# Performance work log

Hardware: AMD Instinct MI355X
Metric: run time of the kernel (lower is better)

Reference implementation:

```python
import jax, jax.numpy as jnp
import numpy as np

# camera / renderer constants (match init_kwargs)
H_IMG, W_IMG = 720, 1280
RR = 2
HS, WS = H_IMG // RR, W_IMG // RR  # 360, 640 ray grid
FX, FY, CX, CY = 600.0, 600.0, 640.0, 360.0
NEAR, FAR = 0.0, 1.5
NS = 10            # N_samples
SHARP = 1000.0
TAU = 100.0
N_SQ = 8
SQRT3 = 3.0 ** 0.5
EPS = 1e-6


def _make_rays():
    # replicates DepthRenderer.get_ray_points with identity camera_pose
    lw = jnp.linspace(0.0, W_IMG - 1, WS)
    lh = jnp.linspace(0.0, H_IMG - 1, HS)
    i, j = jnp.meshgrid(lw, lh)  # 'xy' indexing -> (HS, WS), i varies along width
    dirs = jnp.stack([(i - CX) / FX, -(j - CY) / FY, -jnp.ones_like(i)], -1)
    dirs = dirs / jnp.linalg.norm(dirs, axis=-1, keepdims=True)
    # camera_pose R = I, then right-multiplied by diag(1,-1,-1) in __init__
    R_flip = jnp.diag(jnp.array([1.0, -1.0, -1.0], jnp.float32))
    rays_d = jnp.einsum('hwk,jk->hwj', dirs, R_flip)
    rays_d = rays_d / jnp.linalg.norm(rays_d, axis=-1, keepdims=True)
    rays_o = jnp.zeros(3, jnp.float32)
    return rays_d.astype(jnp.float32), rays_o


def setup_inputs() -> dict:
    key = jax.random.key(0)
    k1, k2, k3, k4, k5 = jax.random.split(key, 5)
    rays_d, rays_o = _make_rays()
    t = jnp.linspace(-1.0, 1.0, NS).astype(jnp.float32)
    # random valid rotations via QR (det fixed to +1; 3x3 so global sign flip negates det)
    A = jax.random.normal(k1, (N_SQ, 3, 3))
    Q, _ = jnp.linalg.qr(A)
    Q = Q * jnp.sign(jnp.linalg.det(Q))[:, None, None]
    pos_xy = jax.random.uniform(k2, (N_SQ, 2), minval=-0.3, maxval=0.3)
    pos_z = jax.random.uniform(k3, (N_SQ, 1), minval=0.5, maxval=1.2)
    pos = jnp.concatenate([pos_xy, pos_z], -1)
    poses = jnp.tile(jnp.eye(4, dtype=jnp.float32)[None], (N_SQ, 1, 1))
    poses = poses.at[:, :3, :3].set(Q).at[:, :3, 3].set(pos)
    sizes = jax.random.uniform(k4, (N_SQ, 3), minval=0.05, maxval=0.15)
    eps12 = jax.random.uniform(k5, (N_SQ, 2), minval=0.3, maxval=1.5)
    params = jnp.concatenate([sizes, eps12], -1).astype(jnp.float32)
    return {"sq_poses": poses.astype(jnp.float32), "sq_params": params,
            "rays_d": rays_d, "rays_o": rays_o, "t": t}


def _sq_F(loc, params):
    # superquadric inside-outside function; F == 1 on the surface
    a = params[:, 0:3][:, None, None, None, :]        # (n,1,1,1,3)
    e1 = params[:, 3][:, None, None, None]
    e2 = params[:, 4][:, None, None, None]
    X = jnp.abs(loc) / a + EPS                        # (n,H,W,S,3)
    f = (X[..., 0] ** (2.0 / e2) + X[..., 1] ** (2.0 / e2)) ** (e2 / e1) \
        + X[..., 2] ** (2.0 / e1)
    return f ** e1


def _forward(sq_poses, sq_params, rays_d, rays_o, t):
    sizes = sq_params[:, 0:3]                         # (n,3)
    R = sq_poses[:, :3, :3]                           # (n,3,3)
    p = sq_poses[:, :3, 3]                            # (n,3)
    # rays into unit-sphere frame of each SQ: R^T d / sizes, renormalized
    td = jnp.einsum('nkj,hwk->nhwj', R, rays_d) / sizes[:, None, None, :]
    td = td / jnp.linalg.norm(td, axis=-1, keepdims=True)   # (n,H,W,3)
    tc = jnp.einsum('nkj,nk->nj', R, rays_o - p) / sizes    # (n,3)
    proj = jnp.abs(jnp.sum(tc[:, None, None, :] * td, -1, keepdims=True))
    cen = tc[:, None, None, :] + proj * td            # closest point on ray (n,H,W,3)
    dist = jnp.linalg.norm(cen, axis=-1)              # (n,H,W)
    mask = dist < SQRT3
    hcl = jnp.sqrt(jnp.maximum(3.0 - dist ** 2, 1e-12))  # half chord length
    # (n,H,W,NS,3) samples in unit frame, then back to world
    pts_loc = cen[..., None, :] + (hcl[..., None] * t)[..., None] * td[..., None, :]
    pts_w = jnp.einsum('nij,nhwsj->nhwsi', R, pts_loc * sizes[:, None, None, None, :]) \
        + p[:, None, None, None, :]
    near_pt = jnp.broadcast_to((rays_o + rays_d * NEAR)[None, :, :, None, :],
                               (N_SQ, HS, WS, 1, 3))
    far_pt = jnp.broadcast_to((rays_o + rays_d * FAR)[None, :, :, None, :],
                              (N_SQ, HS, WS, 1, 3))
    pts = jnp.concatenate([near_pt, pts_w, far_pt], axis=3)  # (n,H,W,NS+2,3)
    # SDF of each SQ's own samples (equivalent to the torch valid_indices select)
    loc = jnp.einsum('nji,nhwsj->nhwsi', R, pts - p[:, None, None, None, :])
    F = _sq_F(loc, sq_params)                         # (n,H,W,NS+2)
    occ = jax.nn.sigmoid(SHARP * (1.0 - F))
    vis = jnp.exp(-TAU * jnp.cumsum(occ, axis=-1))
    dt = jnp.linalg.norm(jnp.diff(pts, axis=-2), axis=-1)    # (n,H,W,NS+1)
    cen_vis = 0.5 * (vis[..., :-1] + vis[..., 1:])           # midpoint rule
    depth_valid = jnp.sum(cen_vis * dt, axis=-1) + NEAR
    depth = jnp.where(mask, depth_valid, FAR)                # (n,H,W)
    return jnp.min(depth, axis=0)                            # depth_render: (H,W)


def reference(sq_poses, sq_params, rays_d, rays_o, t):
    return _forward(sq_poses, sq_params, rays_d, rays_o, t)
```

## Files before the change

### kernel.cpp

```cpp
#include <hip/hip_runtime.h>

constexpr int NPIX = 360 * 640;
constexpr int NSQ = 8, NSAMP = 10;
constexpr float FARV = 1.5f;
constexpr float SHARPV = 1000.0f;
constexpr float TAU2 = 100.0f * 1.44269504f;
constexpr float DT9 = 2.0f / 9.0f;

struct SQT {
  float A[9];
  float tc[3];
  float ie1, ie2, c21, Kq;
  float thr;
  float vis0;
};

__device__ __forceinline__ float lf_eval(float q0, float q1, float q2,
                                         float ie1, float ie2, float c21) {
  const float y0 = fmaf(q0, q0, 1e-12f);
  const float y1 = fmaf(q1, q1, 1e-12f);
  const float y2 = fmaf(q2, q2, 1e-12f);
  const float la = ie2 * __builtin_amdgcn_logf(y0);
  const float lb = ie2 * __builtin_amdgcn_logf(y1);
  const float lc = ie1 * __builtin_amdgcn_logf(y2);
  const float mab = fmaxf(la, lb), nab = fminf(la, lb);
  const float lab = mab + __builtin_amdgcn_logf(1.0f + __builtin_amdgcn_exp2f(nab - mab));
  const float lg = c21 * lab;
  const float mf = fmaxf(lg, lc), nf = fminf(lg, lc);
  return mf + __builtin_amdgcn_logf(1.0f + __builtin_amdgcn_exp2f(nf - mf));
}

__global__ __launch_bounds__(64) void depth_kernel(
    const float* __restrict__ poses, const float* __restrict__ params,
    const float* __restrict__ rays_d, const float* __restrict__ rays_o,
    float* __restrict__ out)
{
  __shared__ SQT sq[NSQ];
  const int tid = threadIdx.x;

  if (tid < NSQ) {
    const int n = tid;
    const float* P = poses + n * 16;
    const float* par = params + n * 5;
    const float is0 = 1.0f / par[0], is1 = 1.0f / par[1], is2 = 1.0f / par[2];
    const float e1 = par[3], e2 = par[4];
    SQT q;
    q.A[0] = P[0] * is0;  q.A[1] = P[1] * is1;  q.A[2] = P[2]  * is2;
    q.A[3] = P[4] * is0;  q.A[4] = P[5] * is1;  q.A[5] = P[6]  * is2;
    q.A[6] = P[8] * is0;  q.A[7] = P[9] * is1;  q.A[8] = P[10] * is2;
    const float d0 = rays_o[0] - P[3], d1 = rays_o[1] - P[7], d2 = rays_o[2] - P[11];
    q.tc[0] = q.A[0] * d0 + q.A[3] * d1 + q.A[6] * d2;
    q.tc[1] = q.A[1] * d0 + q.A[4] * d1 + q.A[7] * d2;
    q.tc[2] = q.A[2] * d0 + q.A[5] * d1 + q.A[8] * d2;
    q.ie1 = 1.0f / e1; q.ie2 = 1.0f / e2; q.c21 = e2 * q.ie1;
    q.Kq = SHARPV * e1;
    const float c = __builtin_amdgcn_exp2f(1.0f - e2);
    const float V1 = (e1 < 1.0f) ? __builtin_amdgcn_exp2f(1.0f - e1) : 1.0f;
    float V2;
    if (e1 < 0.999f) {
      const float cp = __builtin_amdgcn_exp2f((1.0f - e2) / (1.0f - e1));
      V2 = __builtin_amdgcn_exp2f((1.0f - e1) * __builtin_amdgcn_logf(1.0f + cp));
    } else {
      V2 = fmaxf(c, 1.0f);
    }
    q.thr = 1.02f * fmaxf(V1, V2);
    const float lf0 = lf_eval(q.tc[0], q.tc[1], q.tc[2], q.ie1, q.ie2, q.c21);
    const float occ0 = __builtin_amdgcn_rcpf(1.0f + __builtin_amdgcn_exp2f(q.Kq * lf0));
    q.vis0 = __builtin_amdgcn_exp2f(-TAU2 * occ0);
    sq[n] = q;
  }
  __syncthreads();

  const int pix = blockIdx.x * 64 + tid;
  const float rd0 = rays_d[pix * 3 + 0];
  const float rd1 = rays_d[pix * 3 + 1];
  const float rd2 = rays_d[pix * 3 + 2];

  float m = FARV;

  for (int n = 0; n < NSQ; n++) {
    const SQT& q = sq[n];
    const float w0 = q.A[0] * rd0 + q.A[3] * rd1 + q.A[6] * rd2;
    const float w1 = q.A[1] * rd0 + q.A[4] * rd1 + q.A[7] * rd2;
    const float w2 = q.A[2] * rd0 + q.A[5] * rd1 + q.A[8] * rd2;
    const float tc0 = q.tc[0], tc1 = q.tc[1], tc2 = q.tc[2];

    const float lam2 = w0 * w0 + w1 * w1 + w2 * w2;
    const float dd = tc0 * w0 + tc1 * w1 + tc2 * w2;
    const float pb = fabsf(dd) * __builtin_amdgcn_rcpf(lam2);
    const float ce0 = fmaf(pb, w0, tc0);
    const float ce1 = fmaf(pb, w1, tc1);
    const float ce2 = fmaf(pb, w2, tc2);
    const float dist2 = ce0 * ce0 + ce1 * ce1 + ce2 * ce2;
    const bool hit = dist2 < q.thr;
    if (!__any(hit)) continue;

    const float hb = sqrtf(fmaxf(3.0f - dist2, 1e-12f)) * rsqrtf(lam2);
    const float ie1 = q.ie1, ie2 = q.ie2, c21 = q.c21, Kq = q.Kq;

    float ev[NSAMP + 1];
#pragma unroll
    for (int k = 0; k <= NSAMP; k++) {
      const float b = (k < NSAMP) ? fmaf(fmaf((float)k, DT9, -1.0f), hb, pb) : FARV;
      const float lf = lf_eval(fmaf(b, w0, tc0), fmaf(b, w1, tc1), fmaf(b, w2, tc2),
                               ie1, ie2, c21);
      const float occ = __builtin_amdgcn_rcpf(1.0f + __builtin_amdgcn_exp2f(Kq * lf));
      ev[k] = __builtin_amdgcn_exp2f(-TAU2 * occ);
    }

    float v = q.vis0;
    float vn = v * ev[0];
    float depth = (v + vn) * fabsf(pb - hb);
    v = vn;
    float mid = 0.0f;
#pragma unroll
    for (int k = 1; k < NSAMP; k++) { vn = v * ev[k]; mid += v + vn; v = vn; }
    depth += mid * (hb * DT9);
    vn = v * ev[NSAMP];
    depth += (v + vn) * fabsf(FARV - pb - hb);
    depth *= 0.5f;

    m = fminf(m, hit ? depth : FARV);
  }

  out[pix] = m;
}

extern "C" void kernel_launch(void* const* d_in, const int* in_sizes, int n_in,
                              void* d_out, int out_size, void* d_ws, size_t ws_size,
                              hipStream_t stream) {
  const float* poses  = (const float*)d_in[0];
  const float* params = (const float*)d_in[1];
  const float* rays_d = (const float*)d_in[2];
  const float* rays_o = (const float*)d_in[3];

  depth_kernel<<<NPIX / 64, 64, 0, stream>>>(
      poses, params, rays_d, rays_o, (float*)d_out);
}
```

Before: 12.67 us.

## Split into hit-compaction pass and compacted per-pair body kernel

Replaces the single per-pixel kernel with a hit test that writes (pixel, superquadric) pairs through a global atomic counter, followed by a grid-stride kernel that evaluates only those pairs and merges depths with integer atomicMin. This removes wave divergence, where whole wavefronts ran the expensive sampling loop when only some lanes hit. The cost is a memset, two extra launches, contention on one global atomic counter, scattered reads of rays_d, and atomics on the output. If the workspace is too small, the code falls back to the original kernel.

```diff
diff --git a/kernel.cpp b/kernel.cpp
--- a/kernel.cpp
+++ b/kernel.cpp
@@ -30,52 +30,149 @@
   return mf + __builtin_amdgcn_logf(1.0f + __builtin_amdgcn_exp2f(nf - mf));
 }
 
-__global__ __launch_bounds__(64) void depth_kernel(
+__device__ __forceinline__ SQT make_sqt(const float* __restrict__ P,
+                                        const float* __restrict__ par,
+                                        const float* __restrict__ rays_o) {
+  const float is0 = 1.0f / par[0], is1 = 1.0f / par[1], is2 = 1.0f / par[2];
+  const float e1 = par[3], e2 = par[4];
+  SQT q;
+  q.A[0] = P[0] * is0;  q.A[1] = P[1] * is1;  q.A[2] = P[2]  * is2;
+  q.A[3] = P[4] * is0;  q.A[4] = P[5] * is1;  q.A[5] = P[6]  * is2;
+  q.A[6] = P[8] * is0;  q.A[7] = P[9] * is1;  q.A[8] = P[10] * is2;
+  const float d0 = rays_o[0] - P[3], d1 = rays_o[1] - P[7], d2 = rays_o[2] - P[11];
+  q.tc[0] = q.A[0] * d0 + q.A[3] * d1 + q.A[6] * d2;
+  q.tc[1] = q.A[1] * d0 + q.A[4] * d1 + q.A[7] * d2;
+  q.tc[2] = q.A[2] * d0 + q.A[5] * d1 + q.A[8] * d2;
+  q.ie1 = 1.0f / e1; q.ie2 = 1.0f / e2; q.c21 = e2 * q.ie1;
+  q.Kq = SHARPV * e1;
+  const float c = __builtin_amdgcn_exp2f(1.0f - e2);
+  const float V1 = (e1 < 1.0f) ? __builtin_amdgcn_exp2f(1.0f - e1) : 1.0f;
+  float V2;
+  if (e1 < 0.999f) {
+    const float cp = __builtin_amdgcn_exp2f((1.0f - e2) / (1.0f - e1));
+    V2 = __builtin_amdgcn_exp2f((1.0f - e1) * __builtin_amdgcn_logf(1.0f + cp));
+  } else {
+    V2 = fmaxf(c, 1.0f);
+  }
+  q.thr = 1.02f * fmaxf(V1, V2);
+  const float lf0 = lf_eval(q.tc[0], q.tc[1], q.tc[2], q.ie1, q.ie2, q.c21);
+  const float occ0 = __builtin_amdgcn_rcpf(1.0f + __builtin_amdgcn_exp2f(q.Kq * lf0));
+  q.vis0 = __builtin_amdgcn_exp2f(-TAU2 * occ0);
+  return q;
+}
+
+__global__ __launch_bounds__(256) void hit_kernel(
+    const float* __restrict__ poses, const float* __restrict__ params,
+    const float* __restrict__ rays_d, const float* __restrict__ rays_o,
+    float* __restrict__ out, unsigned int* __restrict__ cnt,
+    SQT* __restrict__ tab, unsigned int* __restrict__ pairs)
+{
+  __shared__ SQT sq[NSQ];
+  const int tid = threadIdx.x;
+  if (tid < NSQ) {
+    SQT q = make_sqt(poses + tid * 16, params + tid * 5, rays_o);
+    sq[tid] = q;
+    if (blockIdx.x == 0) tab[tid] = q;
+  }
+  __syncthreads();
+
+  const int pix = blockIdx.x * 256 + tid;
+  const float rd0 = rays_d[pix * 3 + 0];
+  const float rd1 = rays_d[pix * 3 + 1];
+  const float rd2 = rays_d[pix * 3 + 2];
+  out[pix] = FARV;
+
+#pragma unroll
+  for (int n = 0; n < NSQ; n++) {
+    const SQT& q = sq[n];
+    const float w0 = q.A[0] * rd0 + q.A[3] * rd1 + q.A[6] * rd2;
+    const float w1 = q.A[1] * rd0 + q.A[4] * rd1 + q.A[7] * rd2;
+    const float w2 = q.A[2] * rd0 + q.A[5] * rd1 + q.A[8] * rd2;
+    const float lam2 = w0 * w0 + w1 * w1 + w2 * w2;
+    const float dd = q.tc[0] * w0 + q.tc[1] * w1 + q.tc[2] * w2;
+    const float pb = fabsf(dd) * __builtin_amdgcn_rcpf(lam2);
+    const float ce0 = fmaf(pb, w0, q.tc[0]);
+    const float ce1 = fmaf(pb, w1, q.tc[1]);
+    const float ce2 = fmaf(pb, w2, q.tc[2]);
+    const float dist2 = ce0 * ce0 + ce1 * ce1 + ce2 * ce2;
+    if (dist2 < q.thr) {
+      const unsigned idx = atomicAdd(cnt, 1u);
+      pairs[idx] = ((unsigned)pix << 3) | (unsigned)n;
+    }
+  }
+}
+
+__global__ __launch_bounds__(256) void body_kernel(
+    const float* __restrict__ rays_d, const SQT* __restrict__ tab,
+    const unsigned int* __restrict__ pairs, const unsigned int* __restrict__ cnt,
+    int* __restrict__ out)
+{
+  const unsigned count = *cnt;
+  const unsigned stride = gridDim.x * 256;
+  for (unsigned i = blockIdx.x * 256 + threadIdx.x; i < count; i += stride) {
+    const unsigned pr = pairs[i];
+    const int pix = (int)(pr >> 3);
+    const int n = (int)(pr & 7u);
+    const SQT q = tab[n];
+
+    const float rd0 = rays_d[pix * 3 + 0];
+    const float rd1 = rays_d[pix * 3 + 1];
+    const float rd2 = rays_d[pix * 3 + 2];
+    const float w0 = q.A[0] * rd0 + q.A[3] * rd1 + q.A[6] * rd2;
+    const float w1 = q.A[1] * rd0 + q.A[4] * rd1 + q.A[7] * rd2;
+    const float w2 = q.A[2] * rd0 + q.A[5] * rd1 + q.A[8] * rd2;
+    const float tc0 = q.tc[0], tc1 = q.tc[1], tc2 = q.tc[2];
+
+    const float lam2 = w0 * w0 + w1 * w1 + w2 * w2;
+    const float dd = tc0 * w0 + tc1 * w1 + tc2 * w2;
+    const float pb = fabsf(dd) * __builtin_amdgcn_rcpf(lam2);
+    const float ce0 = fmaf(pb, w0, tc0);
+    const float ce1 = fmaf(pb, w1, tc1);
+    const float ce2 = fmaf(pb, w2, tc2);
+    const float dist2 = ce0 * ce0 + ce1 * ce1 + ce2 * ce2;
+    const float hb = sqrtf(fmaxf(3.0f - dist2, 1e-12f)) * rsqrtf(lam2);
+    const float ie1 = q.ie1, ie2 = q.ie2, c21 = q.c21, Kq = q.Kq;
+
+    float ev[NSAMP + 1];
+#pragma unroll
+    for (int k = 0; k <= NSAMP; k++) {
+      const float b = (k < NSAMP) ? fmaf(fmaf((float)k, DT9, -1.0f), hb, pb) : FARV;
+      const float lf = lf_eval(fmaf(b, w0, tc0), fmaf(b, w1, tc1), fmaf(b, w2, tc2),
+                               ie1, ie2, c21);
+      const float occ = __builtin_amdgcn_rcpf(1.0f + __builtin_amdgcn_exp2f(Kq * lf));
+      ev[k] = __builtin_amdgcn_exp2f(-TAU2 * occ);
+    }
+
+    float v = q.vis0;
+    float vn = v * ev[0];
+    float depth = (v + vn) * fabsf(pb - hb);
+    v = vn;
+    float mid = 0.0f;
+#pragma unroll
+    for (int k = 1; k < NSAMP; k++) { vn = v * ev[k]; mid += v + vn; v = vn; }
+    depth += mid * (hb * DT9);
+    vn = v * ev[NSAMP];
+    depth += (v + vn) * fabsf(FARV - pb - hb);
+    depth *= 0.5f;
+
+    atomicMin(out + pix, __float_as_int(depth));
+  }
+}
+
+__global__ __launch_bounds__(64) void depth_kernel_fb(
     const float* __restrict__ poses, const float* __restrict__ params,
     const float* __restrict__ rays_d, const float* __restrict__ rays_o,
     float* __restrict__ out)
 {
   __shared__ SQT sq[NSQ];
   const int tid = threadIdx.x;
-
-  if (tid < NSQ) {
-    const int n = tid;
-    const float* P = poses + n * 16;
-    const float* par = params + n * 5;
-    const float is0 = 1.0f / par[0], is1 = 1.0f / par[1], is2 = 1.0f / par[2];
-    const float e1 = par[3], e2 = par[4];
-    SQT q;
-    q.A[0] = P[0] * is0;  q.A[1] = P[1] * is1;  q.A[2] = P[2]  * is2;
-    q.A[3] = P[4] * is0;  q.A[4] = P[5] * is1;  q.A[5] = P[6]  * is2;
-    q.A[6] = P[8] * is0;  q.A[7] = P[9] * is1;  q.A[8] = P[10] * is2;
-    const float d0 = rays_o[0] - P[3], d1 = rays_o[1] - P[7], d2 = rays_o[2] - P[11];
-    q.tc[0] = q.A[0] * d0 + q.A[3] * d1 + q.A[6] * d2;
-    q.tc[1] = q.A[1] * d0 + q.A[4] * d1 + q.A[7] * d2;
-    q.tc[2] = q.A[2] * d0 + q.A[5] * d1 + q.A[8] * d2;
-    q.ie1 = 1.0f / e1; q.ie2 = 1.0f / e2; q.c21 = e2 * q.ie1;
-    q.Kq = SHARPV * e1;
-    const float c = __builtin_amdgcn_exp2f(1.0f - e2);
-    const float V1 = (e1 < 1.0f) ? __builtin_amdgcn_exp2f(1.0f - e1) : 1.0f;
-    float V2;
-    if (e1 < 0.999f) {
-      const float cp = __builtin_amdgcn_exp2f((1.0f - e2) / (1.0f - e1));
-      V2 = __builtin_amdgcn_exp2f((1.0f - e1) * __builtin_amdgcn_logf(1.0f + cp));
-    } else {
-      V2 = fmaxf(c, 1.0f);
-    }
-    q.thr = 1.02f * fmaxf(V1, V2);
-    const float lf0 = lf_eval(q.tc[0], q.tc[1], q.tc[2], q.ie1, q.ie2, q.c21);
-    const float occ0 = __builtin_amdgcn_rcpf(1.0f + __builtin_amdgcn_exp2f(q.Kq * lf0));
-    q.vis0 = __builtin_amdgcn_exp2f(-TAU2 * occ0);
-    sq[n] = q;
-  }
+  if (tid < NSQ) sq[tid] = make_sqt(poses + tid * 16, params + tid * 5, rays_o);
   __syncthreads();
 
   const int pix = blockIdx.x * 64 + tid;
   const float rd0 = rays_d[pix * 3 + 0];
   const float rd1 = rays_d[pix * 3 + 1];
   const float rd2 = rays_d[pix * 3 + 2];
-
   float m = FARV;
 
   for (int n = 0; n < NSQ; n++) {
@@ -84,7 +181,6 @@
     const float w1 = q.A[1] * rd0 + q.A[4] * rd1 + q.A[7] * rd2;
     const float w2 = q.A[2] * rd0 + q.A[5] * rd1 + q.A[8] * rd2;
     const float tc0 = q.tc[0], tc1 = q.tc[1], tc2 = q.tc[2];
-
     const float lam2 = w0 * w0 + w1 * w1 + w2 * w2;
     const float dd = tc0 * w0 + tc1 * w1 + tc2 * w2;
     const float pb = fabsf(dd) * __builtin_amdgcn_rcpf(lam2);
@@ -94,20 +190,16 @@
     const float dist2 = ce0 * ce0 + ce1 * ce1 + ce2 * ce2;
     const bool hit = dist2 < q.thr;
     if (!__any(hit)) continue;
-
     const float hb = sqrtf(fmaxf(3.0f - dist2, 1e-12f)) * rsqrtf(lam2);
-    const float ie1 = q.ie1, ie2 = q.ie2, c21 = q.c21, Kq = q.Kq;
-
     float ev[NSAMP + 1];
 #pragma unroll
     for (int k = 0; k <= NSAMP; k++) {
       const float b = (k < NSAMP) ? fmaf(fmaf((float)k, DT9, -1.0f), hb, pb) : FARV;
       const float lf = lf_eval(fmaf(b, w0, tc0), fmaf(b, w1, tc1), fmaf(b, w2, tc2),
-                               ie1, ie2, c21);
-      const float occ = __builtin_amdgcn_rcpf(1.0f + __builtin_amdgcn_exp2f(Kq * lf));
+                               q.ie1, q.ie2, q.c21);
+      const float occ = __builtin_amdgcn_rcpf(1.0f + __builtin_amdgcn_exp2f(q.Kq * lf));
       ev[k] = __builtin_amdgcn_exp2f(-TAU2 * occ);
     }
-
     float v = q.vis0;
     float vn = v * ev[0];
     float depth = (v + vn) * fabsf(pb - hb);
@@ -119,10 +211,8 @@
     vn = v * ev[NSAMP];
     depth += (v + vn) * fabsf(FARV - pb - hb);
     depth *= 0.5f;
-
     m = fminf(m, hit ? depth : FARV);
   }
-
   out[pix] = m;
 }
 
@@ -134,6 +224,17 @@
   const float* rays_d = (const float*)d_in[2];
   const float* rays_o = (const float*)d_in[3];
 
-  depth_kernel<<<NPIX / 64, 64, 0, stream>>>(
-      poses, params, rays_d, rays_o, (float*)d_out);
-}
+  const size_t need = 1024 + sizeof(unsigned int) * (size_t)NSQ * NPIX;
+  if (ws_size >= need) {
+    unsigned int* cnt   = (unsigned int*)d_ws;
+    SQT* tab            = (SQT*)((char*)d_ws + 64);
+    unsigned int* pairs = (unsigned int*)((char*)d_ws + 1024);
+    hipMemsetAsync(d_ws, 0, 4, stream);
+    hit_kernel<<<NPIX / 256, 256, 0, stream>>>(
+        poses, params, rays_d, rays_o, (float*)d_out, cnt, tab, pairs);
+    body_kernel<<<1024, 256, 0, stream>>>(rays_d, tab, pairs, cnt, (int*)d_out);
+  } else {
+    depth_kernel_fb<<<NPIX / 64, 64, 0, stream>>>(
+        poses, params, rays_d, rays_o, (float*)d_out);
+  }
+}
```

Measured after the change: 32.14 us. 154% more time.

## Compact hit (pixel, superquadric) pairs per wave to remove divergent evaluation

Applied to the files above, without the earlier changes.

Each thread first tests its ray against all 8 superquadrics and uses ballot and popcount to append the hit (pixel, SQ) pairs to a shared-memory list. The wave then processes that list densely, one pair per lane, and merges depths with an integer atomicMin into a shared per-pixel minimum. This removes idle lanes when only some lanes in a wave hit a given SQ. It adds shared-memory traffic, LDS atomics and an extra barrier, and the integer min assumes depths are non-negative.

```diff
diff --git a/kernel.cpp b/kernel.cpp
--- a/kernel.cpp
+++ b/kernel.cpp
@@ -30,59 +30,92 @@
   return mf + __builtin_amdgcn_logf(1.0f + __builtin_amdgcn_exp2f(nf - mf));
 }
 
+__device__ __forceinline__ SQT make_sqt(const float* __restrict__ P,
+                                        const float* __restrict__ par,
+                                        const float* __restrict__ rays_o) {
+  const float is0 = 1.0f / par[0], is1 = 1.0f / par[1], is2 = 1.0f / par[2];
+  const float e1 = par[3], e2 = par[4];
+  SQT q;
+  q.A[0] = P[0] * is0;  q.A[1] = P[1] * is1;  q.A[2] = P[2]  * is2;
+  q.A[3] = P[4] * is0;  q.A[4] = P[5] * is1;  q.A[5] = P[6]  * is2;
+  q.A[6] = P[8] * is0;  q.A[7] = P[9] * is1;  q.A[8] = P[10] * is2;
+  const float d0 = rays_o[0] - P[3], d1 = rays_o[1] - P[7], d2 = rays_o[2] - P[11];
+  q.tc[0] = q.A[0] * d0 + q.A[3] * d1 + q.A[6] * d2;
+  q.tc[1] = q.A[1] * d0 + q.A[4] * d1 + q.A[7] * d2;
+  q.tc[2] = q.A[2] * d0 + q.A[5] * d1 + q.A[8] * d2;
+  q.ie1 = 1.0f / e1; q.ie2 = 1.0f / e2; q.c21 = e2 * q.ie1;
+  q.Kq = SHARPV * e1;
+  const float c = __builtin_amdgcn_exp2f(1.0f - e2);
+  const float V1 = (e1 < 1.0f) ? __builtin_amdgcn_exp2f(1.0f - e1) : 1.0f;
+  float V2;
+  if (e1 < 0.999f) {
+    const float cp = __builtin_amdgcn_exp2f((1.0f - e2) / (1.0f - e1));
+    V2 = __builtin_amdgcn_exp2f((1.0f - e1) * __builtin_amdgcn_logf(1.0f + cp));
+  } else {
+    V2 = fmaxf(c, 1.0f);
+  }
+  q.thr = 1.02f * fmaxf(V1, V2);
+  const float lf0 = lf_eval(q.tc[0], q.tc[1], q.tc[2], q.ie1, q.ie2, q.c21);
+  const float occ0 = __builtin_amdgcn_rcpf(1.0f + __builtin_amdgcn_exp2f(q.Kq * lf0));
+  q.vis0 = __builtin_amdgcn_exp2f(-TAU2 * occ0);
+  return q;
+}
+
 __global__ __launch_bounds__(64) void depth_kernel(
     const float* __restrict__ poses, const float* __restrict__ params,
     const float* __restrict__ rays_d, const float* __restrict__ rays_o,
     float* __restrict__ out)
 {
   __shared__ SQT sq[NSQ];
+  __shared__ float rdx[64], rdy[64], rdz[64];
+  __shared__ unsigned short list[64 * NSQ];
+  __shared__ int dmin[64];
+
   const int tid = threadIdx.x;
-
-  if (tid < NSQ) {
-    const int n = tid;
-    const float* P = poses + n * 16;
-    const float* par = params + n * 5;
-    const float is0 = 1.0f / par[0], is1 = 1.0f / par[1], is2 = 1.0f / par[2];
-    const float e1 = par[3], e2 = par[4];
-    SQT q;
-    q.A[0] = P[0] * is0;  q.A[1] = P[1] * is1;  q.A[2] = P[2]  * is2;
-    q.A[3] = P[4] * is0;  q.A[4] = P[5] * is1;  q.A[5] = P[6]  * is2;
-    q.A[6] = P[8] * is0;  q.A[7] = P[9] * is1;  q.A[8] = P[10] * is2;
-    const float d0 = rays_o[0] - P[3], d1 = rays_o[1] - P[7], d2 = rays_o[2] - P[11];
-    q.tc[0] = q.A[0] * d0 + q.A[3] * d1 + q.A[6] * d2;
-    q.tc[1] = q.A[1] * d0 + q.A[4] * d1 + q.A[7] * d2;
-    q.tc[2] = q.A[2] * d0 + q.A[5] * d1 + q.A[8] * d2;
-    q.ie1 = 1.0f / e1; q.ie2 = 1.0f / e2; q.c21 = e2 * q.ie1;
-    q.Kq = SHARPV * e1;
-    const float c = __builtin_amdgcn_exp2f(1.0f - e2);
-    const float V1 = (e1 < 1.0f) ? __builtin_amdgcn_exp2f(1.0f - e1) : 1.0f;
-    float V2;
-    if (e1 < 0.999f) {
-      const float cp = __builtin_amdgcn_exp2f((1.0f - e2) / (1.0f - e1));
-      V2 = __builtin_amdgcn_exp2f((1.0f - e1) * __builtin_amdgcn_logf(1.0f + cp));
-    } else {
-      V2 = fmaxf(c, 1.0f);
-    }
-    q.thr = 1.02f * fmaxf(V1, V2);
-    const float lf0 = lf_eval(q.tc[0], q.tc[1], q.tc[2], q.ie1, q.ie2, q.c21);
-    const float occ0 = __builtin_amdgcn_rcpf(1.0f + __builtin_amdgcn_exp2f(q.Kq * lf0));
-    q.vis0 = __builtin_amdgcn_exp2f(-TAU2 * occ0);
-    sq[n] = q;
-  }
-  __syncthreads();
+  if (tid < NSQ) sq[tid] = make_sqt(poses + tid * 16, params + tid * 5, rays_o);
 
   const int pix = blockIdx.x * 64 + tid;
   const float rd0 = rays_d[pix * 3 + 0];
   const float rd1 = rays_d[pix * 3 + 1];
   const float rd2 = rays_d[pix * 3 + 2];
+  rdx[tid] = rd0; rdy[tid] = rd1; rdz[tid] = rd2;
+  dmin[tid] = __float_as_int(FARV);
+  __syncthreads();
 
-  float m = FARV;
-
+  int H = 0;
+#pragma unroll
   for (int n = 0; n < NSQ; n++) {
     const SQT& q = sq[n];
     const float w0 = q.A[0] * rd0 + q.A[3] * rd1 + q.A[6] * rd2;
     const float w1 = q.A[1] * rd0 + q.A[4] * rd1 + q.A[7] * rd2;
     const float w2 = q.A[2] * rd0 + q.A[5] * rd1 + q.A[8] * rd2;
+    const float lam2 = w0 * w0 + w1 * w1 + w2 * w2;
+    const float dd = q.tc[0] * w0 + q.tc[1] * w1 + q.tc[2] * w2;
+    const float pb = fabsf(dd) * __builtin_amdgcn_rcpf(lam2);
+    const float ce0 = fmaf(pb, w0, q.tc[0]);
+    const float ce1 = fmaf(pb, w1, q.tc[1]);
+    const float ce2 = fmaf(pb, w2, q.tc[2]);
+    const float dist2 = ce0 * ce0 + ce1 * ce1 + ce2 * ce2;
+    const bool hit = dist2 < q.thr;
+    const unsigned long long b = __ballot(hit);
+    if (hit) {
+      const int pos = H + __popcll(b & ((1ull << tid) - 1ull));
+      list[pos] = (unsigned short)(tid | (n << 6));
+    }
+    H += __popcll(b);
+  }
+  __syncthreads();
+
+  for (int j = tid; j < H; j += 64) {
+    const int e = list[j];
+    const int src = e & 63;
+    const int n = e >> 6;
+    const SQT& q = sq[n];
+    const float urd0 = rdx[src], urd1 = rdy[src], urd2 = rdz[src];
+
+    const float w0 = q.A[0] * urd0 + q.A[3] * urd1 + q.A[6] * urd2;
+    const float w1 = q.A[1] * urd0 + q.A[4] * urd1 + q.A[7] * urd2;
+    const float w2 = q.A[2] * urd0 + q.A[5] * urd1 + q.A[8] * urd2;
     const float tc0 = q.tc[0], tc1 = q.tc[1], tc2 = q.tc[2];
 
     const float lam2 = w0 * w0 + w1 * w1 + w2 * w2;
@@ -92,9 +125,6 @@
     const float ce1 = fmaf(pb, w1, tc1);
     const float ce2 = fmaf(pb, w2, tc2);
     const float dist2 = ce0 * ce0 + ce1 * ce1 + ce2 * ce2;
-    const bool hit = dist2 < q.thr;
-    if (!__any(hit)) continue;
-
     const float hb = sqrtf(fmaxf(3.0f - dist2, 1e-12f)) * rsqrtf(lam2);
     const float ie1 = q.ie1, ie2 = q.ie2, c21 = q.c21, Kq = q.Kq;
 
@@ -120,10 +150,11 @@
     depth += (v + vn) * fabsf(FARV - pb - hb);
     depth *= 0.5f;
 
-    m = fminf(m, hit ? depth : FARV);
+    atomicMin(&dmin[src], __float_as_int(depth));
   }
+  __syncthreads();
 
-  out[pix] = m;
+  out[pix] = __int_as_float(dmin[tid]);
 }
 
 extern "C" void kernel_launch(void* const* d_in, const int* in_sizes, int n_in,
```

After: 12.50 us. Within noise of the previous version (-1.3%).
